# Optimization experiments

Measured on AMD Instinct MI355X. Metric: run time of the kernel, lower is better.

## Reference

```python
import jax, jax.numpy as jnp
import numpy as np

HEADS = 8
DIM_HEAD = 64
SCALE = DIM_HEAD ** -0.5


def setup_inputs() -> dict:
    key = jax.random.key(0)
    ks = jax.random.split(key, 7)
    b, n, m = 2, 4096, 4096
    query_dim, context_dim, inner = 1024, 768, HEADS * DIM_HEAD
    s = 0.02
    return {
        "x": jax.random.normal(ks[0], (b, n, query_dim), jnp.float32),
        "context": jax.random.normal(ks[1], (b, m, context_dim), jnp.float32),
        "Wq": jax.random.normal(ks[2], (query_dim, inner), jnp.float32) * s,
        "Wk": jax.random.normal(ks[3], (context_dim, inner), jnp.float32) * s,
        "Wv": jax.random.normal(ks[4], (context_dim, inner), jnp.float32) * s,
        "Wo": jax.random.normal(ks[5], (inner, query_dim), jnp.float32) * s,
        "bo": jnp.zeros((query_dim,), jnp.float32),
    }


def reference(x, context, Wq, Wk, Wv, Wo, bo):
    b, n, _ = x.shape
    m = context.shape[1]
    # projections (no bias), split heads: b n (h d) -> b n h d
    q = (x @ Wq).reshape(b, n, HEADS, DIM_HEAD)
    k = (context @ Wk).reshape(b, m, HEADS, DIM_HEAD)
    v = (context @ Wv).reshape(b, m, HEADS, DIM_HEAD)
    # fp32 QK^T (ATTN_PRECISION='fp32' path), full [b,h,n,m] scores
    sim = jnp.einsum("bihd,bjhd->bhij", q.astype(jnp.float32), k.astype(jnp.float32)) * SCALE
    attn = jax.nn.softmax(sim, axis=-1).astype(v.dtype)
    out = jnp.einsum("bhij,bjhd->bihd", attn, v).reshape(b, n, HEADS * DIM_HEAD)
    # to_out: Linear with bias (dropout=0 is identity)
    return out @ Wo + bo
```

## Files before the change

### kernel.cpp

```cpp
#include <hip/hip_runtime.h>
#include <hip/hip_bf16.h>
#include <cmath>
#include <cstdint>


using bf16_t = __hip_bfloat16;
typedef __bf16 bf16x8 __attribute__((ext_vector_type(8)));
typedef float  f32x4  __attribute__((ext_vector_type(4)));
typedef float  f32x16 __attribute__((ext_vector_type(16)));

static constexpr int BATCH = 2;
static constexpr int NQ    = 4096;
static constexpr int NKV   = 4096;
static constexpr int NH    = 8;
static constexpr int DH    = 64;
static constexpr int INNER = NH * DH;
static constexpr int QDIM  = 1024;
static constexpr int CDIM  = 768;
static constexpr float QSCALE = 0.125f * 1.4426950408889634f;

#define MFMA_BF16(a, b, c) __builtin_amdgcn_mfma_f32_16x16x32_bf16((a), (b), (c), 0, 0, 0)
#define MFMA32_BF16(a, b, c) __builtin_amdgcn_mfma_f32_32x32x16_bf16((a), (b), (c), 0, 0, 0)

__device__ __forceinline__ float fast_exp2(float x) {
  return __builtin_amdgcn_exp2f(x);
}

__device__ __forceinline__ void gload16(const bf16_t* g, bf16_t* l) {
  __builtin_amdgcn_global_load_lds((__attribute__((address_space(1))) void*)(g),
                                   (__attribute__((address_space(3))) void*)(l),
                                   16, 0, 0);
}

__device__ __forceinline__ uint32_t pk2(float lo, float hi) {
  __hip_bfloat16 a = __float2bfloat16(lo), b = __float2bfloat16(hi);
  union { unsigned short s[2]; uint32_t u; } x;
  x.s[0] = *(unsigned short*)&a;
  x.s[1] = *(unsigned short*)&b;
  return x.u;
}

__device__ __forceinline__ void pl32swap(uint32_t& a, uint32_t& b) {
  asm volatile("v_permlane32_swap_b32 %0, %1" : "+v"(a), "+v"(b));
}

__device__ __forceinline__ bf16x8 frag4(uint32_t w0, uint32_t w1, uint32_t w2, uint32_t w3) {
  union { uint32_t w[4]; bf16x8 f; } u;
  u.w[0] = w0; u.w[1] = w1; u.w[2] = w2; u.w[3] = w3;
  return u.f;
}

__global__ __launch_bounds__(256) void cast2_kernel(const float* __restrict__ x,
                                                    bf16_t* __restrict__ xb, int xn8,
                                                    const float* __restrict__ c,
                                                    bf16_t* __restrict__ cb, int cn8) {
  int id = blockIdx.x * 256 + threadIdx.x;
  const float* in;
  bf16_t* out;
  if (id < xn8) {
    in = x; out = xb;
  } else {
    id -= xn8;
    if (id >= cn8) return;
    in = c; out = cb;
  }
  float4 a = ((const float4*)in)[2 * id];
  float4 b = ((const float4*)in)[2 * id + 1];
  bf16_t t[8] = {__float2bfloat16(a.x), __float2bfloat16(a.y), __float2bfloat16(a.z),
                 __float2bfloat16(a.w), __float2bfloat16(b.x), __float2bfloat16(b.y),
                 __float2bfloat16(b.z), __float2bfloat16(b.w)};
  ((uint4*)out)[id] = *(const uint4*)t;
}

__global__ __launch_bounds__(256) void wtrans4_kernel(const float* __restrict__ Wq,
                                                      const float* __restrict__ Wk,
                                                      const float* __restrict__ Wv,
                                                      const float* __restrict__ Wo,
                                                      bf16_t* __restrict__ WqT,
                                                      bf16_t* __restrict__ WkvT,
                                                      bf16_t* __restrict__ WoT) {
  __shared__ float tile[32][33];
  const float* W;
  bf16_t* WT;
  int K, N;
  switch (blockIdx.z) {
    case 0: W = Wq; WT = WqT; K = QDIM; N = INNER; break;
    case 1: W = Wk; WT = WkvT; K = CDIM; N = INNER; break;
    case 2: W = Wv; WT = WkvT + (size_t)INNER * CDIM; K = CDIM; N = INNER; break;
    default: W = Wo; WT = WoT; K = INNER; N = QDIM; break;
  }
  const int bn = blockIdx.x * 32, bk = blockIdx.y * 32;
  if (bn >= N || bk >= K) return;
  const int tx = threadIdx.x & 31, ty = threadIdx.x >> 5;
  for (int yy = ty; yy < 32; yy += 8)
    tile[yy][tx] = W[(size_t)(bk + yy) * N + bn + tx];
  __syncthreads();
  for (int yy = ty; yy < 32; yy += 8)
    WT[(size_t)(bn + yy) * K + bk + tx] = __float2bfloat16(tile[tx][yy]);
}

__device__ __forceinline__ void gemm128_core(const bf16_t* __restrict__ A,
                                             const bf16_t* __restrict__ WT, int K,
                                             int m0, int n0, int tid,
                                             f32x4 (&acc)[4][4],
                                             bf16_t (*As)[128][32],
                                             bf16_t (*Bs)[128][32]) {
  const int lane = tid & 63, wave = tid >> 6;
  const int lane15 = lane & 15, quad = lane >> 4;
  const int wm = (wave >> 1) * 64, wn = (wave & 1) * 64;
  const int srow = tid >> 2;
  const int scol = ((tid & 3) ^ ((srow >> 1) & 3)) * 8;
  const bf16_t* aptr = A + (size_t)(m0 + srow) * K + scol;
  const bf16_t* bptr = WT + (size_t)(n0 + srow) * K + scol;
  bf16_t* const ab = &As[0][wave * 16][0];
  bf16_t* const bb = &Bs[0][wave * 16][0];
  constexpr int BUF = 128 * 32;

  auto stage = [&](int t) {
    const int c = (t % 3) * BUF;
    const bf16_t* as = aptr + t * 32;
    const bf16_t* bs = bptr + t * 32;
    gload16(as, ab + c);
    gload16(as + (size_t)64 * K, ab + c + 64 * 32);
    gload16(bs, bb + c);
    gload16(bs + (size_t)64 * K, bb + c + 64 * 32);
  };

  const int T = K / 32;
  stage(0);
  stage(1);
  for (int t = 0; t < T; ++t) {
    const int cur = t % 3;
    if (t < T - 1) {
      asm volatile("s_waitcnt vmcnt(4)" ::: "memory");
    } else {
      asm volatile("s_waitcnt vmcnt(0)" ::: "memory");
    }
    asm volatile("s_barrier" ::: "memory");
    if (t + 2 < T) stage(t + 2);
    bf16x8 af[4], bfr[4];
#pragma unroll
    for (int i = 0; i < 4; ++i) {
      const int row = wm + i * 16 + lane15;
      af[i] = *reinterpret_cast<const bf16x8*>(
          &As[cur][0][0] + row * 32 + ((quad * 8) ^ (((row >> 1) & 3) * 8)));
    }
#pragma unroll
    for (int j = 0; j < 4; ++j) {
      const int row = wn + j * 16 + lane15;
      bfr[j] = *reinterpret_cast<const bf16x8*>(
          &Bs[cur][0][0] + row * 32 + ((quad * 8) ^ (((row >> 1) & 3) * 8)));
    }
#pragma unroll
    for (int i = 0; i < 4; ++i)
#pragma unroll
      for (int j = 0; j < 4; ++j) acc[i][j] = MFMA_BF16(af[i], bfr[j], acc[i][j]);
  }
}

__global__ __launch_bounds__(256, 3) void qkv_gemm_kernel(const bf16_t* __restrict__ xb,
                                                          const bf16_t* __restrict__ ctxb,
                                                          const bf16_t* __restrict__ WqT,
                                                          const bf16_t* __restrict__ WkvT,
                                                          bf16_t* __restrict__ qob,
                                                          bf16_t* __restrict__ kb,
                                                          bf16_t* __restrict__ vtb) {
  __shared__ __align__(16) bf16_t As[3][128][32];
  __shared__ __align__(16) bf16_t Bs[3][128][32];
  const int tid = threadIdx.x;
  const bool isq = blockIdx.y < 4;
  const bf16_t* A  = isq ? xb : ctxb;
  const bf16_t* WT = isq ? WqT : WkvT;
  const int K  = isq ? QDIM : CDIM;
  const int m0 = blockIdx.x * 128;
  const int n0 = (isq ? blockIdx.y : blockIdx.y - 4) * 128;

  const f32x4 vzero = {0.f, 0.f, 0.f, 0.f};
  f32x4 acc[4][4];
  for (int i = 0; i < 4; ++i)
    for (int j = 0; j < 4; ++j) acc[i][j] = vzero;

  gemm128_core(A, WT, K, m0, n0, tid, acc, As, Bs);

  const int lane = tid & 63, wave = tid >> 6;
  const int lane15 = lane & 15, quad = lane >> 4;
  const int wm = (wave >> 1) * 64, wn = (wave & 1) * 64;
  for (int i = 0; i < 4; ++i) {
    int gm = m0 + wm + i * 16 + quad * 4;
    for (int j = 0; j < 4; ++j) {
      int gn = n0 + wn + j * 16 + lane15;
      for (int r = 0; r < 4; ++r) {
        float v = acc[i][j][r];
        if (isq) {
          qob[(size_t)(gm + r) * INNER + gn] = __float2bfloat16(v * QSCALE);
        } else if (gn < INNER) {
          kb[(size_t)(gm + r) * INNER + gn] = __float2bfloat16(v);
        } else {
          int gmr = gm + r;
          vtb[((size_t)(gmr >> 12) * INNER + (gn - INNER)) * (size_t)NKV +
              (gmr & 4095)] = __float2bfloat16(v);
        }
      }
    }
  }
}

__global__ __launch_bounds__(256, 3) void out_gemm_kernel(const bf16_t* __restrict__ A,
                                                          const bf16_t* __restrict__ WT,
                                                          float* __restrict__ C,
                                                          const float* __restrict__ bias) {
  __shared__ __align__(16) bf16_t As[3][128][32];
  __shared__ __align__(16) bf16_t Bs[3][128][32];
  const int tid = threadIdx.x;
  const int m0 = blockIdx.x * 128, n0 = blockIdx.y * 128;
  constexpr int K = INNER, N = QDIM;

  const f32x4 vzero = {0.f, 0.f, 0.f, 0.f};
  f32x4 acc[4][4];
  for (int i = 0; i < 4; ++i)
    for (int j = 0; j < 4; ++j) acc[i][j] = vzero;

  gemm128_core(A, WT, K, m0, n0, tid, acc, As, Bs);

  const int lane = tid & 63, wave = tid >> 6;
  const int lane15 = lane & 15, quad = lane >> 4;
  const int wm = (wave >> 1) * 64, wn = (wave & 1) * 64;
  float bv[4];
  for (int j = 0; j < 4; ++j) bv[j] = bias[n0 + wn + j * 16 + lane15];
  for (int i = 0; i < 4; ++i) {
    int gm = m0 + wm + i * 16 + quad * 4;
    for (int j = 0; j < 4; ++j) {
      int gn = n0 + wn + j * 16 + lane15;
      for (int r = 0; r < 4; ++r)
        C[(size_t)(gm + r) * N + gn] = acc[i][j][r] + bv[j];
    }
  }
}

__global__ __launch_bounds__(512, 4) void attn_kernel(const bf16_t* Qg ,
                                                      const bf16_t* __restrict__ Kg ,
                                                      const bf16_t* __restrict__ Vtg ,
                                                      bf16_t* Og ) {
  __shared__ __align__(16) char smem[33792];
  auto KsF = (bf16_t(*)[8][512])smem;
  auto VtF = (bf16_t(*)[8][512])(smem + 16384);
  float* scrO = (float*)smem;
  float* scrL = (float*)(smem + 32768);

  const int tid = threadIdx.x;
  const int lane = tid & 63, wave = tid >> 6;
  const int lane31 = lane & 31, hi = lane >> 5;
  const int qg = wave >> 1;
  const int v  = wave & 1;
  const int q0 = blockIdx.x * 128;
  const int h = blockIdx.y;
  const int b = blockIdx.z;

  const size_t qbase  = ((size_t)b * NQ + q0) * INNER + h * DH;
  const size_t kbase  = ((size_t)b * NKV) * INNER + h * DH;
  const size_t vtbase = ((size_t)(b * NH + h) * DH) * NKV;

  bf16x8 qf[4];
#pragma unroll
  for (int kc = 0; kc < 4; ++kc)
    qf[kc] = *reinterpret_cast<const bf16x8*>(
        Qg + qbase + (size_t)(qg * 32 + lane31) * INNER + kc * 16 + hi * 8);

  bf16x8 ones;
#pragma unroll
  for (int i = 0; i < 8; ++i) ones[i] = (__bf16)1.0f;

  f32x16 acc_o[2];
  f32x16 acc_l;
  for (int i = 0; i < 16; ++i) { acc_o[0][i] = 0.f; acc_o[1][i] = 0.f; acc_l[i] = 0.f; }

  const int skv = (wave >> 2) * 32, skc = (wave & 3) * 16;
  const int sdt = ((wave >> 1) & 1) * 32, skb = (wave & 1) * 16;
  auto kaddr = [&](int kv0) {
    return Kg + kbase + (size_t)(kv0 + skv + lane31) * INNER + skc + hi * 8;
  };
  auto vaddr = [&](int kv0) {
    return Vtg + vtbase + (size_t)(sdt + lane31) * NKV + kv0 + skv + skb + hi * 8;
  };
  uint4 kr = *(const uint4*)kaddr(0);
  uint4 vr = *(const uint4*)vaddr(0);

  constexpr int T = NKV / 64;
  for (int t = 0; t < T; ++t) {
    const int cur = t & 1;
    *(uint4*)&KsF[cur][wave][lane * 8] = kr;
    *(uint4*)&VtF[cur][wave][lane * 8] = vr;
    __syncthreads();

    if (t + 1 < T) {
      kr = *(const uint4*)kaddr((t + 1) * 64);
      vr = *(const uint4*)vaddr((t + 1) * 64);
    }

    f32x16 st;
    for (int i = 0; i < 16; ++i) st[i] = 0.f;
    __builtin_amdgcn_s_setprio(1);
#pragma unroll
    for (int kc = 0; kc < 4; ++kc) {
      bf16x8 kf = *reinterpret_cast<const bf16x8*>(&KsF[cur][v * 4 + kc][lane * 8]);
      st = MFMA32_BF16(kf, qf[kc], st);
    }
    __builtin_amdgcn_s_setprio(0);

    uint32_t c0 = pk2(fast_exp2(st[0]),  fast_exp2(st[1]));
    uint32_t c1 = pk2(fast_exp2(st[2]),  fast_exp2(st[3]));
    uint32_t c2 = pk2(fast_exp2(st[4]),  fast_exp2(st[5]));
    uint32_t c3 = pk2(fast_exp2(st[6]),  fast_exp2(st[7]));
    uint32_t c4 = pk2(fast_exp2(st[8]),  fast_exp2(st[9]));
    uint32_t c5 = pk2(fast_exp2(st[10]), fast_exp2(st[11]));
    uint32_t c6 = pk2(fast_exp2(st[12]), fast_exp2(st[13]));
    uint32_t c7 = pk2(fast_exp2(st[14]), fast_exp2(st[15]));
    pl32swap(c0, c2);
    pl32swap(c1, c3);
    pl32swap(c4, c6);
    pl32swap(c5, c7);
    bf16x8 pf0 = frag4(c0, c1, c2, c3);
    bf16x8 pf1 = frag4(c4, c5, c6, c7);

    __builtin_amdgcn_s_setprio(1);
    acc_l = MFMA32_BF16(pf0, ones, acc_l);
    acc_l = MFMA32_BF16(pf1, ones, acc_l);
#pragma unroll
    for (int dt = 0; dt < 2; ++dt) {
      bf16x8 vf0 = *reinterpret_cast<const bf16x8*>(&VtF[cur][v * 4 + dt * 2 + 0][lane * 8]);
      bf16x8 vf1 = *reinterpret_cast<const bf16x8*>(&VtF[cur][v * 4 + dt * 2 + 1][lane * 8]);
      acc_o[dt] = MFMA32_BF16(pf0, vf0, acc_o[dt]);
      acc_o[dt] = MFMA32_BF16(pf1, vf1, acc_o[dt]);
    }
    __builtin_amdgcn_s_setprio(0);
  }

  __syncthreads();
  if (v == 1) {
#pragma unroll
    for (int dt = 0; dt < 2; ++dt)
      for (int r = 0; r < 16; ++r)
        scrO[((qg * 2 + dt) * 16 + r) * 64 + lane] = acc_o[dt][r];
    if (lane31 == 0)
      for (int r = 0; r < 16; ++r) scrL[(qg * 2 + hi) * 16 + r] = acc_l[r];
  }
  __syncthreads();
  if (v == 0) {
    for (int r = 0; r < 16; ++r) {
      float lt = acc_l[r] + scrL[(qg * 2 + hi) * 16 + r];
      float inv = 1.f / lt;
      int qrow = qg * 32 + (r & 3) + 8 * (r >> 2) + 4 * hi;
      for (int dt = 0; dt < 2; ++dt) {
        float o = acc_o[dt][r] + scrO[((qg * 2 + dt) * 16 + r) * 64 + lane];
        Og[qbase + (size_t)qrow * INNER + dt * 32 + lane31] = __float2bfloat16(o * inv);
      }
    }
  }
}

extern "C" void kernel_launch(void* const* d_in, const int* in_sizes, int n_in,
                              void* d_out, int out_size, void* d_ws, size_t ws_size,
                              hipStream_t stream) {
  (void)in_sizes; (void)n_in; (void)out_size; (void)ws_size;
  const float* x   = (const float*)d_in[0];
  const float* ctx = (const float*)d_in[1];
  const float* Wq  = (const float*)d_in[2];
  const float* Wk  = (const float*)d_in[3];
  const float* Wv  = (const float*)d_in[4];
  const float* Wo  = (const float*)d_in[5];
  const float* bo  = (const float*)d_in[6];
  float* out = (float*)d_out;

  char* ws = (char*)d_ws;
  size_t off = 0;
  auto take = [&](size_t nelem) { bf16_t* p = (bf16_t*)(ws + off); off += nelem * 2; return p; };
  bf16_t* WqT  = take((size_t)INNER * QDIM);
  bf16_t* WkvT = take((size_t)(2 * INNER) * CDIM);
  bf16_t* WoT  = take((size_t)QDIM * INNER);
  bf16_t* qob  = take((size_t)BATCH * NQ * INNER);
  bf16_t* kb   = take((size_t)BATCH * NKV * INNER);
  bf16_t* vtb  = take((size_t)BATCH * INNER * NKV);

  bf16_t* xb   = (bf16_t*)d_out;
  bf16_t* ctxb = xb + (size_t)BATCH * NQ * QDIM;

  const int M = BATCH * NQ;
  const int xN8 = BATCH * NQ * QDIM / 8, cN8 = BATCH * NKV * CDIM / 8;

  cast2_kernel<<<(xN8 + cN8 + 255) / 256, 256, 0, stream>>>(x, xb, xN8, ctx, ctxb, cN8);
  wtrans4_kernel<<<dim3(32, 32, 4), 256, 0, stream>>>(Wq, Wk, Wv, Wo, WqT, WkvT, WoT);

  qkv_gemm_kernel<<<dim3(M / 128, 12), 256, 0, stream>>>(xb, ctxb, WqT, WkvT, qob, kb, vtb);

  attn_kernel<<<dim3(NQ / 128, NH, BATCH), 512, 0, stream>>>(qob, kb, vtb, qob);

  out_gemm_kernel<<<dim3(M / 128, QDIM / 128), 256, 0, stream>>>(qob, WoT, out, bo);
}
```

Before: 248.9 us.

## Compute V transposed directly via swapped GEMM operands and flatten projection grid

The projection kernel now uses a 1D grid of 768 blocks: Q tiles, K tiles, and V tiles. The V tiles compute Wv^T·ctx^T, swapping the operands so the output lands in the transposed V layout with coalesced stores instead of scattered strided writes. Block order also groups tiles sharing the same A rows, which may help cache reuse. The attention kernel seeds the first QK MFMA with a zero vector rather than zero-initialising the accumulator inside the loop.

```diff
diff --git a/kernel.cpp b/kernel.cpp
--- a/kernel.cpp
+++ b/kernel.cpp
@@ -158,22 +158,33 @@
   }
 }
 
-__global__ __launch_bounds__(256, 3) void qkv_gemm_kernel(const bf16_t* __restrict__ xb,
-                                                          const bf16_t* __restrict__ ctxb,
-                                                          const bf16_t* __restrict__ WqT,
-                                                          const bf16_t* __restrict__ WkvT,
-                                                          bf16_t* __restrict__ qob,
-                                                          bf16_t* __restrict__ kb,
-                                                          bf16_t* __restrict__ vtb) {
+__global__ __launch_bounds__(256, 3) void proj_gemm_kernel(const bf16_t* __restrict__ xb,
+                                                           const bf16_t* __restrict__ ctxb,
+                                                           const bf16_t* __restrict__ WqT,
+                                                           const bf16_t* __restrict__ WkvT,
+                                                           bf16_t* __restrict__ qob,
+                                                           bf16_t* __restrict__ kb,
+                                                           bf16_t* __restrict__ vtb) {
   __shared__ __align__(16) bf16_t As[3][128][32];
   __shared__ __align__(16) bf16_t Bs[3][128][32];
   const int tid = threadIdx.x;
-  const bool isq = blockIdx.y < 4;
-  const bf16_t* A  = isq ? xb : ctxb;
-  const bf16_t* WT = isq ? WqT : WkvT;
-  const int K  = isq ? QDIM : CDIM;
-  const int m0 = blockIdx.x * 128;
-  const int n0 = (isq ? blockIdx.y : blockIdx.y - 4) * 128;
+  const int bid = blockIdx.x;
+  const bf16_t *A, *WT;
+  int K, m0, n0, mode;
+  if (bid < 256) {
+    mode = 0; A = xb; WT = WqT; K = QDIM;
+    m0 = (bid >> 2) * 128; n0 = (bid & 3) * 128;
+  } else if (bid < 512) {
+    const int i = bid - 256;
+    mode = 1; A = ctxb; WT = WkvT; K = CDIM;
+    m0 = (i >> 2) * 128; n0 = (i & 3) * 128;
+  } else {
+    const int i = bid - 512;
+    mode = 2; A = WkvT + (size_t)INNER * CDIM;
+    WT = ctxb; K = CDIM;
+    m0 = (i & 3) * 128;
+    n0 = (i >> 2) * 128;
+  }
 
   const f32x4 vzero = {0.f, 0.f, 0.f, 0.f};
   f32x4 acc[4][4];
@@ -191,14 +202,13 @@
       int gn = n0 + wn + j * 16 + lane15;
       for (int r = 0; r < 4; ++r) {
         float v = acc[i][j][r];
-        if (isq) {
+        if (mode == 0) {
           qob[(size_t)(gm + r) * INNER + gn] = __float2bfloat16(v * QSCALE);
-        } else if (gn < INNER) {
+        } else if (mode == 1) {
           kb[(size_t)(gm + r) * INNER + gn] = __float2bfloat16(v);
         } else {
-          int gmr = gm + r;
-          vtb[((size_t)(gmr >> 12) * INNER + (gn - INNER)) * (size_t)NKV +
-              (gmr & 4095)] = __float2bfloat16(v);
+          vtb[((size_t)(gn >> 12) * INNER + (gm + r)) * (size_t)NKV + (gn & 4095)] =
+              __float2bfloat16(v);
         }
       }
     }
@@ -270,6 +280,10 @@
 #pragma unroll
   for (int i = 0; i < 8; ++i) ones[i] = (__bf16)1.0f;
 
+  f32x16 z16;
+#pragma unroll
+  for (int i = 0; i < 16; ++i) z16[i] = 0.f;
+
   f32x16 acc_o[2];
   f32x16 acc_l;
   for (int i = 0; i < 16; ++i) { acc_o[0][i] = 0.f; acc_o[1][i] = 0.f; acc_l[i] = 0.f; }
@@ -297,11 +311,11 @@
       vr = *(const uint4*)vaddr((t + 1) * 64);
     }
 
-    f32x16 st;
-    for (int i = 0; i < 16; ++i) st[i] = 0.f;
     __builtin_amdgcn_s_setprio(1);
-#pragma unroll
-    for (int kc = 0; kc < 4; ++kc) {
+    bf16x8 kf0 = *reinterpret_cast<const bf16x8*>(&KsF[cur][v * 4 + 0][lane * 8]);
+    f32x16 st = MFMA32_BF16(kf0, qf[0], z16);
+#pragma unroll
+    for (int kc = 1; kc < 4; ++kc) {
       bf16x8 kf = *reinterpret_cast<const bf16x8*>(&KsF[cur][v * 4 + kc][lane * 8]);
       st = MFMA32_BF16(kf, qf[kc], st);
     }
@@ -390,7 +404,7 @@
   cast2_kernel<<<(xN8 + cN8 + 255) / 256, 256, 0, stream>>>(x, xb, xN8, ctx, ctxb, cN8);
   wtrans4_kernel<<<dim3(32, 32, 4), 256, 0, stream>>>(Wq, Wk, Wv, Wo, WqT, WkvT, WoT);
 
-  qkv_gemm_kernel<<<dim3(M / 128, 12), 256, 0, stream>>>(xb, ctxb, WqT, WkvT, qob, kb, vtb);
+  proj_gemm_kernel<<<768, 256, 0, stream>>>(xb, ctxb, WqT, WkvT, qob, kb, vtb);
 
   attn_kernel<<<dim3(NQ / 128, NH, BATCH), 512, 0, stream>>>(qob, kb, vtb, qob);
 
```

Result: slower. 255.9 us (+2.8%).
